# Kernel tuning notes

Hardware: AMD Instinct MI355X
Metric: run time of the kernel (lower is better)

## Reference

```python
import jax, jax.numpy as jnp
import numpy as np

LN_EPS = 1e-5  # nn.LayerNorm default
N_HEAD = 12


def layer_norm(x, w, b, eps=LN_EPS):
    m = jnp.mean(x, axis=-1, keepdims=True)
    v = jnp.var(x, axis=-1, keepdims=True)
    return (x - m) * jax.lax.rsqrt(v + eps) * w + b


def mha(x, in_proj_w, in_proj_b, out_w, out_b, n_head):
    # x: [B,S,D]; self-attention, q=k=v=x (torch nn.MultiheadAttention math)
    B, S, D = x.shape
    hd = D // n_head
    qkv = x @ in_proj_w.T + in_proj_b              # [B,S,3D]
    q, k, v = jnp.split(qkv, 3, axis=-1)
    q = q.reshape(B, S, n_head, hd)
    k = k.reshape(B, S, n_head, hd)
    v = v.reshape(B, S, n_head, hd)
    scale = 1.0 / jnp.sqrt(jnp.asarray(hd, x.dtype))
    scores = jnp.einsum('bqhd,bkhd->bhqk', q, k) * scale  # [B,H,S,S]
    attn = jax.nn.softmax(scores, axis=-1)
    o = jnp.einsum('bhqk,bkhd->bqhd', attn, v).reshape(B, S, D)
    return o @ out_w.T + out_b


def setup_inputs() -> dict:
    key = jax.random.key(0)
    ks = jax.random.split(key, 8)
    B, S, D = 4, 2048, 768
    d_ff = 4 * D
    sd = 0.02
    return {
        'x': jax.random.normal(ks[0], (B, S, D), jnp.float32),
        'ln1_w': jnp.ones((D,), jnp.float32),
        'ln1_b': jnp.zeros((D,), jnp.float32),
        'in_proj_w': jax.random.normal(ks[1], (3 * D, D), jnp.float32) * sd,
        'in_proj_b': jax.random.normal(ks[2], (3 * D,), jnp.float32) * sd,
        'out_w': jax.random.normal(ks[3], (D, D), jnp.float32) * sd,
        'out_b': jax.random.normal(ks[4], (D,), jnp.float32) * sd,
        'ln2_w': jnp.ones((D,), jnp.float32),
        'ln2_b': jnp.zeros((D,), jnp.float32),
        'fc_w': jax.random.normal(ks[5], (d_ff, D), jnp.float32) * sd,
        'fc_b': jnp.zeros((d_ff,), jnp.float32),
        'proj_w': jax.random.normal(ks[6], (D, d_ff), jnp.float32) * sd,
        'proj_b': jnp.zeros((D,), jnp.float32),
    }


def reference(x, ln1_w, ln1_b, in_proj_w, in_proj_b, out_w, out_b,
              ln2_w, ln2_b, fc_w, fc_b, proj_w, proj_b):
    h = layer_norm(x, ln1_w, ln1_b)
    x = x + mha(h, in_proj_w, in_proj_b, out_w, out_b, N_HEAD)
    h2 = layer_norm(x, ln2_w, ln2_b)
    mlp = jax.nn.gelu(h2 @ fc_w.T + fc_b, approximate=False) @ proj_w.T + proj_b
    return x + mlp
```

## Files before the change

### kernel.cpp

```cpp
#include <hip/hip_runtime.h>
#include <hip/hip_bf16.h>
#include <math.h>

#define D_MODEL 768
#define N_HEADS 12
#define HD 64
#define SEQ 2048
#define BATCH 4
#define M_ROWS 8192
#define D_FF 3072
#define QKV_DIM 2304
#define LN_EPS 1e-5f
#define Q_SCALE 0.18033688011112042f

typedef __attribute__((ext_vector_type(8))) short bf16x8;
typedef __attribute__((ext_vector_type(4))) float f32x4;
typedef __hip_bfloat16 bf16;

__device__ __forceinline__ void store_val(float* p, float v) { *p = v; }
__device__ __forceinline__ void store_val(bf16* p, float v) { *p = __float2bfloat16(v); }

__device__ __forceinline__ unsigned int pack_bf16_pair(float a, float b) {
    unsigned int ua = __builtin_bit_cast(unsigned int, a) + 0x8000u;
    unsigned int ub = __builtin_bit_cast(unsigned int, b) + 0x8000u;
    return __builtin_amdgcn_perm(ub, ua, 0x07060302u);
}

__device__ __forceinline__ void async_load16(const void* g, void* l) {
    __builtin_amdgcn_global_load_lds(
        (const __attribute__((address_space(1))) void*)g,
        (__attribute__((address_space(3))) void*)l, 16, 0, 0);
}

__global__ __launch_bounds__(256) void ln1_cast(
        const float* __restrict__ x, const float* __restrict__ w,
        const float* __restrict__ b, bf16* __restrict__ y,
        const float* __restrict__ s0, bf16* __restrict__ d0, int n0,
        const float* __restrict__ s1, bf16* __restrict__ d1, int n1,
        const float* __restrict__ s2, bf16* __restrict__ d2, int n2,
        const float* __restrict__ s3, bf16* __restrict__ d3, int n3) {
    int t = threadIdx.x;
    if (blockIdx.x >= M_ROWS) {
        int i = (blockIdx.x - M_ROWS) * 256 + t;
        const float* s; bf16* d; int local = i;
        if (local < n0) { s = s0; d = d0; }
        else {
            local -= n0;
            if (local < n1) { s = s1; d = d1; }
            else {
                local -= n1;
                if (local < n2) { s = s2; d = d2; }
                else {
                    local -= n2;
                    if (local >= n3) return;
                    s = s3; d = d3;
                }
            }
        }
        float4 v = ((const float4*)s)[local];
        uint2 pk;
        pk.x = pack_bf16_pair(v.x, v.y);
        pk.y = pack_bf16_pair(v.z, v.w);
        *(uint2*)(d + local * 4) = pk;
        return;
    }
    int row = blockIdx.x;
    const float* xr = x + (size_t)row * D_MODEL;
    bf16* yr = y + (size_t)row * D_MODEL;
    float v0 = xr[t], v1 = xr[t + 256], v2 = xr[t + 512];
    float s  = v0 + v1 + v2;
    float sq = v0 * v0 + v1 * v1 + v2 * v2;
    #pragma unroll
    for (int off = 32; off; off >>= 1) {
        s  += __shfl_xor(s, off);
        sq += __shfl_xor(sq, off);
    }
    __shared__ float ss[4], ssq[4];
    int wave = t >> 6;
    if ((t & 63) == 0) { ss[wave] = s; ssq[wave] = sq; }
    __syncthreads();
    s  = ss[0] + ss[1] + ss[2] + ss[3];
    sq = ssq[0] + ssq[1] + ssq[2] + ssq[3];
    float mean = s * (1.0f / D_MODEL);
    float var  = sq * (1.0f / D_MODEL) - mean * mean;
    float rstd = rsqrtf(var + LN_EPS);
    yr[t]       = __float2bfloat16((v0 - mean) * rstd * w[t]       + b[t]);
    yr[t + 256] = __float2bfloat16((v1 - mean) * rstd * w[t + 256] + b[t + 256]);
    yr[t + 512] = __float2bfloat16((v2 - mean) * rstd * w[t + 512] + b[t + 512]);
}

template <typename OutT>
__global__ __launch_bounds__(256) void ln_kernel(const float* __restrict__ x,
                                                 const float* __restrict__ w,
                                                 const float* __restrict__ b,
                                                 OutT* __restrict__ y) {
    int row = blockIdx.x;
    const float* xr = x + (size_t)row * D_MODEL;
    OutT* yr = y + (size_t)row * D_MODEL;
    int t = threadIdx.x;
    float v0 = xr[t], v1 = xr[t + 256], v2 = xr[t + 512];
    float s  = v0 + v1 + v2;
    float sq = v0 * v0 + v1 * v1 + v2 * v2;
    #pragma unroll
    for (int off = 32; off; off >>= 1) {
        s  += __shfl_xor(s, off);
        sq += __shfl_xor(sq, off);
    }
    __shared__ float ss[4], ssq[4];
    int wave = t >> 6;
    if ((t & 63) == 0) { ss[wave] = s; ssq[wave] = sq; }
    __syncthreads();
    s  = ss[0] + ss[1] + ss[2] + ss[3];
    sq = ssq[0] + ssq[1] + ssq[2] + ssq[3];
    float mean = s * (1.0f / D_MODEL);
    float var  = sq * (1.0f / D_MODEL) - mean * mean;
    float rstd = rsqrtf(var + LN_EPS);
    store_val(yr + t,       (v0 - mean) * rstd * w[t]       + b[t]);
    store_val(yr + t + 256, (v1 - mean) * rstd * w[t + 256] + b[t + 256]);
    store_val(yr + t + 512, (v2 - mean) * rstd * w[t + 512] + b[t + 512]);
}

__device__ __forceinline__ float gelu_fast(float v) {
    float u = v * (0.7978845608f + 0.0356774081f * v * v);
    u = fminf(fmaxf(u, -10.0f), 10.0f);
    float e = __builtin_amdgcn_exp2f(u * 2.8853900818f);
    float th = (e - 1.0f) * __builtin_amdgcn_rcpf(e + 1.0f);
    return 0.5f * v * (1.0f + th);
}

template <int FUSE, typename OutT>
__global__ __launch_bounds__(256) void gemm_mfma(const bf16* __restrict__ A,
                                                 const bf16* __restrict__ W,
                                                 const float* __restrict__ bias,
                                                 const float* __restrict__ resid,
                                                 OutT* __restrict__ C,
                                                 int M, int N, int K) {
    const int BK = 64;
    __shared__ __align__(16) bf16 As[2][128 * BK];
    __shared__ __align__(16) bf16 Bs[2][128 * BK];
    int t = threadIdx.x;
    int wave = t >> 6, lane = t & 63;
    int m_base = blockIdx.y * 128, n_base = blockIdx.x * 128;
    int wm = (wave >> 1) * 64, wn = (wave & 1) * 64;
    int c = lane & 15, rr = lane >> 4;

    f32x4 acc[4][4] = {};

    const bf16* Ag[4]; const bf16* Bg[4];
    int loff[4];
    #pragma unroll
    for (int r = 0; r < 4; r++) {
        int s = r * 256 + t;
        int row = s >> 3, p = s & 7;
        int kc = p ^ (row & 7);
        Ag[r] = A + (size_t)(m_base + row) * K + kc * 8;
        Bg[r] = W + (size_t)(n_base + row) * K + kc * 8;
        loff[r] = (r * 256 + wave * 64) * 8;
    }

    #pragma unroll
    for (int r = 0; r < 4; r++) {
        async_load16(Ag[r], As[0] + loff[r]);
        async_load16(Bg[r], Bs[0] + loff[r]);
    }
    __syncthreads();

    int nk = K / BK;
    for (int ki = 0; ki < nk; ki++) {
        int cur = ki & 1;
        if (ki + 1 < nk) {
            int k0n = (ki + 1) * BK;
            #pragma unroll
            for (int r = 0; r < 4; r++) {
                async_load16(Ag[r] + k0n, As[cur ^ 1] + loff[r]);
                async_load16(Bg[r] + k0n, Bs[cur ^ 1] + loff[r]);
            }
        }

        #pragma unroll
        for (int kk = 0; kk < 2; kk++) {
            int sw = ((kk * 4 + rr) ^ (c & 7)) * 8;
            bf16x8 af[4], bfr[4];
            #pragma unroll
            for (int mi = 0; mi < 4; mi++)
                af[mi] = *(const bf16x8*)&As[cur][(wm + mi * 16 + c) * BK + sw];
            #pragma unroll
            for (int ni = 0; ni < 4; ni++)
                bfr[ni] = *(const bf16x8*)&Bs[cur][(wn + ni * 16 + c) * BK + sw];
            #pragma unroll
            for (int mi = 0; mi < 4; mi++)
                #pragma unroll
                for (int ni = 0; ni < 4; ni++)
                    acc[mi][ni] = __builtin_amdgcn_mfma_f32_16x16x32_bf16(
                        bfr[ni], af[mi], acc[mi][ni], 0, 0, 0);
        }
        __syncthreads();
    }

    #pragma unroll
    for (int mi = 0; mi < 4; mi++) {
        int m = m_base + wm + mi * 16 + c;
        #pragma unroll
        for (int ni = 0; ni < 4; ni++) {
            int n0 = n_base + wn + ni * 16 + rr * 4;
            float4 bv = *(const float4*)&bias[n0];
            float v0 = acc[mi][ni][0] + bv.x;
            float v1 = acc[mi][ni][1] + bv.y;
            float v2 = acc[mi][ni][2] + bv.z;
            float v3 = acc[mi][ni][3] + bv.w;
            if (FUSE == 1) {
                v0 = gelu_fast(v0); v1 = gelu_fast(v1);
                v2 = gelu_fast(v2); v3 = gelu_fast(v3);
            }
            if (FUSE == 2) {
                float4 rv = *(const float4*)&resid[(size_t)m * N + n0];
                v0 += rv.x; v1 += rv.y; v2 += rv.z; v3 += rv.w;
            }
            if (FUSE == 3 && n0 < 768) {
                v0 *= Q_SCALE; v1 *= Q_SCALE; v2 *= Q_SCALE; v3 *= Q_SCALE;
            }
            OutT* dst = C + (size_t)m * N + n0;
            if (sizeof(OutT) == 4) {
                float4 st = {v0, v1, v2, v3};
                *(float4*)dst = st;
            } else {
                uint2 pk;
                pk.x = pack_bf16_pair(v0, v1);
                pk.y = pack_bf16_pair(v2, v3);
                *(uint2*)dst = pk;
            }
        }
    }
}

__global__ __launch_bounds__(256) void vtrans(const bf16* __restrict__ qkvb,
                                              bf16* __restrict__ vt) {
    __shared__ bf16 T[64 * 72];
    int t = threadIdx.x;
    int s0 = blockIdx.x * 64, h = blockIdx.y, b = blockIdx.z;
    const bf16* src = qkvb + (size_t)(b * SEQ) * QKV_DIM + 2 * D_MODEL + h * HD;
    #pragma unroll
    for (int i = 0; i < 2; i++) {
        int idx = i * 256 + t;
        int sr = idx >> 3, ch = idx & 7;
        uint4 v = *(const uint4*)(src + (size_t)(s0 + sr) * QKV_DIM + ch * 8);
        *(uint4*)&T[sr * 72 + ch * 8] = v;
    }
    __syncthreads();
    int dr = t >> 2, part = t & 3;
    unsigned int w[8];
    #pragma unroll
    for (int i = 0; i < 8; i++) {
        unsigned short a, bsh;
        __builtin_memcpy(&a,   &T[(part * 16 + 2 * i    ) * 72 + dr], 2);
        __builtin_memcpy(&bsh, &T[(part * 16 + 2 * i + 1) * 72 + dr], 2);
        w[i] = (unsigned int)a | ((unsigned int)bsh << 16);
    }
    bf16* dst = vt + ((size_t)((b * N_HEADS + h) * HD + dr)) * SEQ + s0 + part * 16;
    uint4 p0; p0.x = w[0]; p0.y = w[1]; p0.z = w[2]; p0.w = w[3];
    uint4 p1; p1.x = w[4]; p1.y = w[5]; p1.z = w[6]; p1.w = w[7];
    *(uint4*)dst = p0;
    *(uint4*)(dst + 8) = p1;
}

__global__ __launch_bounds__(256) void attn_mfma(const bf16* __restrict__ qkvb,
                                                 const bf16* __restrict__ vt,
                                                 bf16* __restrict__ o) {
    __shared__ __align__(16) bf16 Ks[2 * 64 * 64];
    __shared__ __align__(16) bf16 Vts[2 * 64 * 64];
    __shared__ __align__(16) bf16 Ps[128 * 64];

    int t = threadIdx.x;
    int wave = t >> 6, lane = t & 63;
    int qt = blockIdx.x, h = blockIdx.y, b = blockIdx.z;
    int s0 = qt * 128;
    int wq = wave * 32;
    int c = lane & 15, rr = lane >> 4;
    int cx = c & 7;

    const bf16* qbase  = qkvb + (size_t)b * SEQ * QKV_DIM + h * HD;
    const bf16* kbase  = qbase + D_MODEL;
    const bf16* vtbase = vt + (size_t)((b * N_HEADS + h) * HD) * SEQ;

    #pragma unroll
    for (int r = 0; r < 4; r++) {
        int lin = r * 256 + t;
        int qq = lin >> 3, p = lin & 7;
        int kc = p ^ (qq & 7);
        async_load16(qbase + (size_t)(s0 + qq) * QKV_DIM + kc * 8,
                     Ps + (size_t)(r * 256 + wave * 64) * 8);
    }
    #pragma unroll
    for (int r = 0; r < 2; r++) {
        int row = (r * 256 + t) >> 3;
        int kc = ((r * 256 + t) & 7) ^ (row & 7);
        async_load16(kbase + (size_t)row * QKV_DIM + kc * 8,
                     Ks + (size_t)(r * 256 + wave * 64) * 8);
        async_load16(vtbase + (size_t)row * SEQ + kc * 8,
                     Vts + (size_t)(r * 256 + wave * 64) * 8);
    }
    __syncthreads();

    bf16x8 bq[2][2];
    #pragma unroll
    for (int m = 0; m < 2; m++)
        #pragma unroll
        for (int kk = 0; kk < 2; kk++)
            bq[m][kk] = *(const bf16x8*)&Ps[(wq + m * 16 + c) * 64 + ((kk * 4 + rr) ^ cx) * 8];

    bf16x8 ones;
    #pragma unroll
    for (int i = 0; i < 8; i++) ones[i] = (short)0x3F80;

    f32x4 Oa[2][4] = {};
    f32x4 La[2] = {};

    for (int jt = 0; jt < SEQ; jt += 64) {
        int cur = (jt >> 6) & 1;
        bf16* Kb  = Ks  + cur * 4096;
        bf16* Vtb = Vts + cur * 4096;

        if (jt + 64 < SEQ) {
            bf16* Kn  = Ks  + (cur ^ 1) * 4096;
            bf16* Vtn = Vts + (cur ^ 1) * 4096;
            #pragma unroll
            for (int r = 0; r < 2; r++) {
                int row = (r * 256 + t) >> 3;
                int kc = ((r * 256 + t) & 7) ^ (row & 7);
                async_load16(kbase + (size_t)(jt + 64 + row) * QKV_DIM + kc * 8,
                             Kn + (size_t)(r * 256 + wave * 64) * 8);
                async_load16(vtbase + (size_t)row * SEQ + (jt + 64) + kc * 8,
                             Vtn + (size_t)(r * 256 + wave * 64) * 8);
            }
        }

        f32x4 St[4][2] = {};
        __builtin_amdgcn_s_setprio(1);
        #pragma unroll
        for (int kk = 0; kk < 2; kk++) {
            bf16x8 ak[4];
            #pragma unroll
            for (int jj = 0; jj < 4; jj++)
                ak[jj] = *(const bf16x8*)&Kb[(jj * 16 + c) * 64 + ((kk * 4 + rr) ^ cx) * 8];
            #pragma unroll
            for (int jj = 0; jj < 4; jj++)
                #pragma unroll
                for (int m = 0; m < 2; m++)
                    St[jj][m] = __builtin_amdgcn_mfma_f32_16x16x32_bf16(
                        ak[jj], bq[m][kk], St[jj][m], 0, 0, 0);
        }
        __builtin_amdgcn_s_setprio(0);

        #pragma unroll
        for (int jj = 0; jj < 4; jj++) {
            int off = ((jj * 2 + (rr >> 1)) ^ cx) * 8 + (rr & 1) * 4;
            #pragma unroll
            for (int m = 0; m < 2; m++) {
                float p0 = __builtin_amdgcn_exp2f(St[jj][m][0]);
                float p1 = __builtin_amdgcn_exp2f(St[jj][m][1]);
                float p2 = __builtin_amdgcn_exp2f(St[jj][m][2]);
                float p3 = __builtin_amdgcn_exp2f(St[jj][m][3]);
                uint2 pk;
                pk.x = pack_bf16_pair(p0, p1);
                pk.y = pack_bf16_pair(p2, p3);
                *(uint2*)&Ps[(wq + m * 16 + c) * 64 + off] = pk;
            }
        }

        __builtin_amdgcn_s_setprio(1);
        #pragma unroll
        for (int kk = 0; kk < 2; kk++) {
            bf16x8 ap[2];
            #pragma unroll
            for (int m = 0; m < 2; m++)
                ap[m] = *(const bf16x8*)&Ps[(wq + m * 16 + c) * 64 + ((kk * 4 + rr) ^ cx) * 8];
            #pragma unroll
            for (int m = 0; m < 2; m++)
                La[m] = __builtin_amdgcn_mfma_f32_16x16x32_bf16(
                    ap[m], ones, La[m], 0, 0, 0);
            #pragma unroll
            for (int n = 0; n < 4; n++) {
                bf16x8 bv = *(const bf16x8*)&Vtb[(n * 16 + c) * 64 + ((kk * 4 + rr) ^ cx) * 8];
                #pragma unroll
                for (int m = 0; m < 2; m++)
                    Oa[m][n] = __builtin_amdgcn_mfma_f32_16x16x32_bf16(
                        ap[m], bv, Oa[m][n], 0, 0, 0);
            }
        }
        __builtin_amdgcn_s_setprio(0);

        __syncthreads();
    }

    #pragma unroll
    for (int m = 0; m < 2; m++)
        #pragma unroll
        for (int rg = 0; rg < 4; rg++) {
            float inv = __builtin_amdgcn_rcpf(La[m][rg]);
            int q = s0 + wq + m * 16 + rr * 4 + rg;
            bf16* op = o + (size_t)(b * SEQ + q) * D_MODEL + h * HD;
            #pragma unroll
            for (int n = 0; n < 4; n++)
                op[n * 16 + c] = __float2bfloat16(Oa[m][n][rg] * inv);
        }
}

extern "C" void kernel_launch(void* const* d_in, const int* in_sizes, int n_in,
                              void* d_out, int out_size, void* d_ws, size_t ws_size,
                              hipStream_t stream) {
    const float* x         = (const float*)d_in[0];
    const float* ln1_w     = (const float*)d_in[1];
    const float* ln1_b     = (const float*)d_in[2];
    const float* in_proj_w = (const float*)d_in[3];
    const float* in_proj_b = (const float*)d_in[4];
    const float* out_w     = (const float*)d_in[5];
    const float* out_b     = (const float*)d_in[6];
    const float* ln2_w     = (const float*)d_in[7];
    const float* ln2_b     = (const float*)d_in[8];
    const float* fc_w      = (const float*)d_in[9];
    const float* fc_b      = (const float*)d_in[10];
    const float* proj_w    = (const float*)d_in[11];
    const float* proj_b    = (const float*)d_in[12];

    float* out = (float*)d_out;
    char*  ws  = (char*)d_ws;

    bf16* qkvb = (bf16*)ws;
    bf16* vt   = (bf16*)(ws + 37748736);
    bf16* ff   = (bf16*)ws;
    bf16* h    = (bf16*)(ws + 50331648);
    bf16* o    = (bf16*)(ws + 62914560);
    bf16* wbf  = (bf16*)(ws + 75497472);
    bf16* wqkv_b  = wbf;
    bf16* wout_b  = wqkv_b + (size_t)QKV_DIM * D_MODEL;
    bf16* wfc_b   = wout_b + (size_t)D_MODEL * D_MODEL;
    bf16* wproj_b = wfc_b  + (size_t)D_FF * D_MODEL;

    int n0 = QKV_DIM * D_MODEL / 4, n1 = D_MODEL * D_MODEL / 4;
    int n2 = D_FF * D_MODEL / 4,    n3 = D_MODEL * D_FF / 4;
    int cast_blocks = (n0 + n1 + n2 + n3 + 255) / 256;

    ln1_cast<<<M_ROWS + cast_blocks, 256, 0, stream>>>(
        x, ln1_w, ln1_b, h,
        in_proj_w, wqkv_b, n0, out_w, wout_b, n1, fc_w, wfc_b, n2, proj_w, wproj_b, n3);
    gemm_mfma<3, bf16><<<dim3(QKV_DIM / 128, M_ROWS / 128), 256, 0, stream>>>(
        h, wqkv_b, in_proj_b, nullptr, qkvb, M_ROWS, QKV_DIM, D_MODEL);
    vtrans<<<dim3(SEQ / 64, N_HEADS, BATCH), 256, 0, stream>>>(qkvb, vt);
    attn_mfma<<<dim3(SEQ / 128, N_HEADS, BATCH), 256, 0, stream>>>(qkvb, vt, o);
    gemm_mfma<2, float><<<dim3(D_MODEL / 128, M_ROWS / 128), 256, 0, stream>>>(
        o, wout_b, out_b, x, out, M_ROWS, D_MODEL, D_MODEL);
    ln_kernel<bf16><<<M_ROWS, 256, 0, stream>>>(out, ln2_w, ln2_b, h);
    gemm_mfma<1, bf16><<<dim3(D_FF / 128, M_ROWS / 128), 256, 0, stream>>>(
        h, wfc_b, fc_b, nullptr, ff, M_ROWS, D_FF, D_MODEL);
    gemm_mfma<2, float><<<dim3(D_MODEL / 128, M_ROWS / 128), 256, 0, stream>>>(
        ff, wproj_b, proj_b, out, out, M_ROWS, D_MODEL, D_FF);
}
```

Before: 394.8 us.

## Add 256x128-tile triple-buffered GEMM for QKV and FC projections

Adds a new GEMM kernel with 512 threads, a 256x128 output tile and a three-stage async LDS pipeline. It is used for the QKV and FC1 GEMMs. The larger M tile halves how often the weight tiles are reloaded, and the extra stage gives more load latency hiding. In exchange it uses more LDS per block (about 144KB), so fewer blocks fit per CU and the grid has fewer, larger blocks.

Measured after the change: 414.2 us. 1.05x slower.

```diff
diff --git a/kernel.cpp b/kernel.cpp
--- a/kernel.cpp
+++ b/kernel.cpp
@@ -129,6 +129,123 @@
 }
 
 template <int FUSE, typename OutT>
+__global__ __launch_bounds__(512) void gemm_big(const bf16* __restrict__ A,
+                                                const bf16* __restrict__ W,
+                                                const float* __restrict__ bias,
+                                                OutT* __restrict__ C,
+                                                int M, int N, int K) {
+    const int BK = 64;
+    __shared__ __align__(16) bf16 As[3][256 * 64];
+    __shared__ __align__(16) bf16 Bs[3][128 * 64];
+    int t = threadIdx.x;
+    int wave = t >> 6, lane = t & 63;
+    int m_base = blockIdx.y * 256, n_base = blockIdx.x * 128;
+    int wm = (wave >> 1) * 64;
+    int wn = (wave & 1) * 64;
+    int c = lane & 15, rr = lane >> 4;
+    int cx = c & 7;
+
+    f32x4 acc[4][4] = {};
+
+    const bf16* Ag[4]; const bf16* Bg[2];
+    int Aoff[4], Boff[2];
+    #pragma unroll
+    for (int r = 0; r < 4; r++) {
+        int s = r * 512 + t;
+        int row = s >> 3, p = s & 7;
+        int kc = p ^ (row & 7);
+        Ag[r] = A + (size_t)(m_base + row) * K + kc * 8;
+        Aoff[r] = (r * 512 + wave * 64) * 8;
+    }
+    #pragma unroll
+    for (int r = 0; r < 2; r++) {
+        int s = r * 512 + t;
+        int row = s >> 3, p = s & 7;
+        int kc = p ^ (row & 7);
+        Bg[r] = W + (size_t)(n_base + row) * K + kc * 8;
+        Boff[r] = (r * 512 + wave * 64) * 8;
+    }
+
+    auto STAGE = [&](int kt, int buf) {
+        int k0 = kt * BK;
+        #pragma unroll
+        for (int r = 0; r < 4; r++)
+            async_load16(Ag[r] + k0, (bf16*)As[buf] + Aoff[r]);
+        #pragma unroll
+        for (int r = 0; r < 2; r++)
+            async_load16(Bg[r] + k0, (bf16*)Bs[buf] + Boff[r]);
+    };
+
+    int nk = K / BK;
+    STAGE(0, 0);
+    STAGE(1, 1);
+
+    int cur = 0;
+    for (int ki = 0; ki < nk; ki++) {
+        if (ki < nk - 1) {
+            asm volatile("s_waitcnt vmcnt(6)" ::: "memory");
+        } else {
+            asm volatile("s_waitcnt vmcnt(0)" ::: "memory");
+        }
+        __builtin_amdgcn_s_barrier();
+        __builtin_amdgcn_sched_barrier(0);
+        if (ki + 2 < nk) STAGE(ki + 2, cur == 0 ? 2 : cur - 1);
+
+        const bf16* Ab = As[cur];
+        const bf16* Bb = Bs[cur];
+        #pragma unroll
+        for (int kk = 0; kk < 2; kk++) {
+            int sw = ((kk * 4 + rr) ^ cx) * 8;
+            bf16x8 af[4], bfr[4];
+            #pragma unroll
+            for (int mi = 0; mi < 4; mi++)
+                af[mi] = *(const bf16x8*)&Ab[(wm + mi * 16 + c) * 64 + sw];
+            #pragma unroll
+            for (int ni = 0; ni < 4; ni++)
+                bfr[ni] = *(const bf16x8*)&Bb[(wn + ni * 16 + c) * 64 + sw];
+            #pragma unroll
+            for (int mi = 0; mi < 4; mi++)
+                #pragma unroll
+                for (int ni = 0; ni < 4; ni++)
+                    acc[mi][ni] = __builtin_amdgcn_mfma_f32_16x16x32_bf16(
+                        bfr[ni], af[mi], acc[mi][ni], 0, 0, 0);
+        }
+        cur = cur == 2 ? 0 : cur + 1;
+    }
+
+    #pragma unroll
+    for (int mi = 0; mi < 4; mi++) {
+        int m = m_base + wm + mi * 16 + c;
+        #pragma unroll
+        for (int ni = 0; ni < 4; ni++) {
+            int n0 = n_base + wn + ni * 16 + rr * 4;
+            float4 bv = *(const float4*)&bias[n0];
+            float v0 = acc[mi][ni][0] + bv.x;
+            float v1 = acc[mi][ni][1] + bv.y;
+            float v2 = acc[mi][ni][2] + bv.z;
+            float v3 = acc[mi][ni][3] + bv.w;
+            if (FUSE == 1) {
+                v0 = gelu_fast(v0); v1 = gelu_fast(v1);
+                v2 = gelu_fast(v2); v3 = gelu_fast(v3);
+            }
+            if (FUSE == 3 && n0 < 768) {
+                v0 *= Q_SCALE; v1 *= Q_SCALE; v2 *= Q_SCALE; v3 *= Q_SCALE;
+            }
+            OutT* dst = C + (size_t)m * N + n0;
+            if (sizeof(OutT) == 4) {
+                float4 st = {v0, v1, v2, v3};
+                *(float4*)dst = st;
+            } else {
+                uint2 pk;
+                pk.x = pack_bf16_pair(v0, v1);
+                pk.y = pack_bf16_pair(v2, v3);
+                *(uint2*)dst = pk;
+            }
+        }
+    }
+}
+
+template <int FUSE, typename OutT>
 __global__ __launch_bounds__(256) void gemm_mfma(const bf16* __restrict__ A,
                                                  const bf16* __restrict__ W,
                                                  const float* __restrict__ bias,
@@ -443,15 +560,15 @@
     ln1_cast<<<M_ROWS + cast_blocks, 256, 0, stream>>>(
         x, ln1_w, ln1_b, h,
         in_proj_w, wqkv_b, n0, out_w, wout_b, n1, fc_w, wfc_b, n2, proj_w, wproj_b, n3);
-    gemm_mfma<3, bf16><<<dim3(QKV_DIM / 128, M_ROWS / 128), 256, 0, stream>>>(
-        h, wqkv_b, in_proj_b, nullptr, qkvb, M_ROWS, QKV_DIM, D_MODEL);
+    gemm_big<3, bf16><<<dim3(QKV_DIM / 128, M_ROWS / 256), 512, 0, stream>>>(
+        h, wqkv_b, in_proj_b, qkvb, M_ROWS, QKV_DIM, D_MODEL);
     vtrans<<<dim3(SEQ / 64, N_HEADS, BATCH), 256, 0, stream>>>(qkvb, vt);
     attn_mfma<<<dim3(SEQ / 128, N_HEADS, BATCH), 256, 0, stream>>>(qkvb, vt, o);
     gemm_mfma<2, float><<<dim3(D_MODEL / 128, M_ROWS / 128), 256, 0, stream>>>(
         o, wout_b, out_b, x, out, M_ROWS, D_MODEL, D_MODEL);
     ln_kernel<bf16><<<M_ROWS, 256, 0, stream>>>(out, ln2_w, ln2_b, h);
-    gemm_mfma<1, bf16><<<dim3(D_FF / 128, M_ROWS / 128), 256, 0, stream>>>(
-        h, wfc_b, fc_b, nullptr, ff, M_ROWS, D_FF, D_MODEL);
+    gemm_big<1, bf16><<<dim3(D_FF / 128, M_ROWS / 256), 512, 0, stream>>>(
+        h, wfc_b, fc_b, ff, M_ROWS, D_FF, D_MODEL);
     gemm_mfma<2, float><<<dim3(D_MODEL / 128, M_ROWS / 128), 256, 0, stream>>>(
         ff, wproj_b, proj_b, out, out, M_ROWS, D_MODEL, D_FF);
 }
```

## Pipeline GEMM loads two stages ahead and remap workgroups for XCD locality

Applied to the files above, without the earlier changes.

The GEMM main loop now issues global-to-LDS loads two k-tiles ahead, waiting with explicit vmcnt counters and raw barriers. Each iteration reads all LDS fragments into registers before refilling that buffer, and raises wave priority around the MFMA block. Both the GEMM and attention kernels remap block IDs so that consecutive tiles land on the same XCD (an 8-way chiplet swizzle), aiming for better L2 reuse. The cost is more registers for the fragment arrays and reliance on hand-tuned waitcnt values, and the swizzle assumes the block count divides by 8.

New measurement: 382.8 us. 3.0% less time.

```diff
diff --git a/kernel.cpp b/kernel.cpp
--- a/kernel.cpp
+++ b/kernel.cpp
@@ -140,9 +140,16 @@
     __shared__ __align__(16) bf16 Bs[2][128 * BK];
     int t = threadIdx.x;
     int wave = t >> 6, lane = t & 63;
-    int m_base = blockIdx.y * 128, n_base = blockIdx.x * 128;
+
+    int nbx = gridDim.x;
+    int w0 = blockIdx.x + nbx * blockIdx.y;
+    int cpx = (nbx * gridDim.y) >> 3;
+    int wg = (w0 & 7) * cpx + (w0 >> 3);
+    int m_base = (wg / nbx) * 128, n_base = (wg % nbx) * 128;
+
     int wm = (wave >> 1) * 64, wn = (wave & 1) * 64;
     int c = lane & 15, rr = lane >> 4;
+    int cx = c & 7;
 
     f32x4 acc[4][4] = {};
 
@@ -158,43 +165,56 @@
         loff[r] = (r * 256 + wave * 64) * 8;
     }
 
-    #pragma unroll
-    for (int r = 0; r < 4; r++) {
-        async_load16(Ag[r], As[0] + loff[r]);
-        async_load16(Bg[r], Bs[0] + loff[r]);
-    }
-    __syncthreads();
+    auto STAGE = [&](int kt, int buf) {
+        int k0 = kt * BK;
+        #pragma unroll
+        for (int r = 0; r < 4; r++) {
+            async_load16(Ag[r] + k0, As[buf] + loff[r]);
+            async_load16(Bg[r] + k0, Bs[buf] + loff[r]);
+        }
+    };
 
     int nk = K / BK;
+    STAGE(0, 0);
+    STAGE(1, 1);
+
     for (int ki = 0; ki < nk; ki++) {
         int cur = ki & 1;
-        if (ki + 1 < nk) {
-            int k0n = (ki + 1) * BK;
-            #pragma unroll
-            for (int r = 0; r < 4; r++) {
-                async_load16(Ag[r] + k0n, As[cur ^ 1] + loff[r]);
-                async_load16(Bg[r] + k0n, Bs[cur ^ 1] + loff[r]);
-            }
-        }
-
+        if (ki < nk - 1) {
+            asm volatile("s_waitcnt vmcnt(8)" ::: "memory");
+        } else {
+            asm volatile("s_waitcnt vmcnt(0)" ::: "memory");
+        }
+        __builtin_amdgcn_s_barrier();
+        __builtin_amdgcn_sched_barrier(0);
+
+        bf16x8 af[2][4], bfr[2][4];
         #pragma unroll
         for (int kk = 0; kk < 2; kk++) {
-            int sw = ((kk * 4 + rr) ^ (c & 7)) * 8;
-            bf16x8 af[4], bfr[4];
+            int sw = ((kk * 4 + rr) ^ cx) * 8;
             #pragma unroll
             for (int mi = 0; mi < 4; mi++)
-                af[mi] = *(const bf16x8*)&As[cur][(wm + mi * 16 + c) * BK + sw];
+                af[kk][mi] = *(const bf16x8*)&As[cur][(wm + mi * 16 + c) * BK + sw];
             #pragma unroll
             for (int ni = 0; ni < 4; ni++)
-                bfr[ni] = *(const bf16x8*)&Bs[cur][(wn + ni * 16 + c) * BK + sw];
+                bfr[kk][ni] = *(const bf16x8*)&Bs[cur][(wn + ni * 16 + c) * BK + sw];
+        }
+        asm volatile("s_waitcnt lgkmcnt(0)" ::: "memory");
+        __builtin_amdgcn_s_barrier();
+        __builtin_amdgcn_sched_barrier(0);
+
+        if (ki + 2 < nk) STAGE(ki + 2, cur);
+
+        __builtin_amdgcn_s_setprio(1);
+        #pragma unroll
+        for (int kk = 0; kk < 2; kk++)
             #pragma unroll
             for (int mi = 0; mi < 4; mi++)
                 #pragma unroll
                 for (int ni = 0; ni < 4; ni++)
                     acc[mi][ni] = __builtin_amdgcn_mfma_f32_16x16x32_bf16(
-                        bfr[ni], af[mi], acc[mi][ni], 0, 0, 0);
-        }
-        __syncthreads();
+                        bfr[kk][ni], af[kk][mi], acc[mi][ni], 0, 0, 0);
+        __builtin_amdgcn_s_setprio(0);
     }
 
     #pragma unroll
@@ -272,7 +292,13 @@
 
     int t = threadIdx.x;
     int wave = t >> 6, lane = t & 63;
-    int qt = blockIdx.x, h = blockIdx.y, b = blockIdx.z;
+
+    int w0 = blockIdx.x + 16 * (blockIdx.y + 12 * blockIdx.z);
+    int wg = (w0 & 7) * 96 + (w0 >> 3);
+    int qt = wg & 15;
+    int hb = wg >> 4;
+    int h = hb % 12, b = hb / 12;
+
     int s0 = qt * 128;
     int wq = wave * 32;
     int c = lane & 15, rr = lane >> 4;
```
